# Kernel optimization log

Measured on AMD Instinct MI355X. Metric: run time of the kernel, lower is better.

The kernel has to match this reference:

```python
import jax, jax.numpy as jnp
import numpy as np

N_TOKENS, DIM = 4096, 2048
N_EXPERTS, TOPK, INTER = 32, 4, 1408
ALPHA, LIMIT, LIN_OFFSET = 1.702, 7.0, 1.0


def quick_geglu(h, probs):
    # h: [..., 2*INTER], interleaved gate/up as in the torch code (x[..., ::2], x[..., 1::2])
    gate = jnp.minimum(h[..., ::2], LIMIT)
    up = jnp.clip(h[..., 1::2], -LIMIT, LIMIT)
    glu = gate * jax.nn.sigmoid(ALPHA * gate)
    return glu * (up + LIN_OFFSET) * probs


def setup_inputs() -> dict:
    key = jax.random.key(0)
    k1, k2, k3, k4, k5 = jax.random.split(key, 5)
    x = jax.random.normal(k1, (N_TOKENS, DIM), dtype=jnp.float32)
    token_mask = jnp.ones((N_TOKENS,), dtype=bool)
    w = jax.random.uniform(k2, (N_TOKENS, TOPK), dtype=jnp.float32)
    weights = w / jnp.sum(w, axis=-1, keepdims=True)  # routing probs
    indices = jax.random.randint(k3, (N_TOKENS, TOPK), 0, N_EXPERTS, dtype=jnp.int64)
    gate_and_up_projs = 0.02 * jax.random.normal(k4, (N_EXPERTS, DIM, 2 * INTER), dtype=jnp.float32)
    down_projs = 0.02 * jax.random.normal(k5, (N_EXPERTS, INTER, DIM), dtype=jnp.float32)
    return {"x": x, "token_mask": token_mask, "weights": weights, "indices": indices,
            "gate_and_up_projs": gate_and_up_projs, "down_projs": down_projs}


def _moe_forward(x, weights, gup, down, token_mask, indices):
    N, D = x.shape
    E = gup.shape[0]
    topk = indices.shape[1]
    T = N * topk
    C = 2 * ((T + E - 1) // E)

    # masked tokens get expert id -1 (as in _permute_tokens_for_grouped_mm)
    flat_e = jnp.where(token_mask[:, None], indices, -1).reshape(-1)
    valid = flat_e >= 0
    e_id = jnp.where(valid, flat_e, E).astype(jnp.int32)  # invalid -> overflow group E
    w = jnp.where(valid, weights.reshape(-1).astype(jnp.float32), 0.0)
    tok = jnp.repeat(jnp.arange(N, dtype=jnp.int32), topk)

    # stable sort by expert (permutation step)
    order = jnp.argsort(e_id)
    se, st, sw = e_id[order], tok[order], w[order]

    # rank of each sorted assignment within its expert group
    counts = jnp.bincount(e_id, length=E + 1)
    starts = jnp.concatenate([jnp.zeros((1,), jnp.int32), jnp.cumsum(counts).astype(jnp.int32)])
    rank = jnp.arange(T, dtype=jnp.int32) - starts[se]
    valid_slot = (se < E) & (rank < C)
    dest = jnp.where(valid_slot, se * C + rank, E * C)  # overflow/dump row E*C

    # scatter permuted tokens into padded per-expert buffers [E, C, D]
    xb = jnp.zeros((E * C + 1, D), x.dtype).at[dest].set(x[st])
    pb = jnp.zeros((E * C + 1,), jnp.float32).at[dest].set(sw)
    tb = jnp.full((E * C + 1,), N, jnp.int32).at[dest].set(st)

    xg = xb[:E * C].reshape(E, C, D)
    h = jnp.einsum('ecd,edh->ech', xg, gup)                       # grouped gate+up GEMM
    a = quick_geglu(h, pb[:E * C].reshape(E, C, 1)).astype(x.dtype)  # fused act * probs
    y = jnp.einsum('ech,ehd->ecd', a, down).reshape(E * C, D)      # grouped down GEMM

    # combine: scatter-add back to token positions (empty slots have prob 0 -> y == 0)
    out = jnp.zeros((N + 1, D), x.dtype).at[tb[:E * C]].add(y)
    return out[:N]


def reference(x, token_mask, weights, indices, gate_and_up_projs, down_projs):
    return _moe_forward(x, weights, gate_and_up_projs, down_projs, token_mask, indices)
```

## Files before the change

kernel.cpp:

```cpp
#include <hip/hip_runtime.h>
#include <hip/hip_bf16.h>
#include <cstdint>
#include <cstddef>

#define N_TOKENS  4096
#define DIM       2048
#define N_EXPERTS 32
#define TOPK      4
#define INTER     1408
#define TWO_INTER 2816
#define CAP       1024
#define T_ASSIGN  (N_TOKENS*TOPK)
#define BK        32

typedef __attribute__((ext_vector_type(8))) short short8;
typedef __attribute__((ext_vector_type(4))) float f32x4;

__device__ __forceinline__ unsigned pack_bf16(float a, float b) {
  unsigned ua = __builtin_bit_cast(unsigned, a);
  unsigned ub = __builtin_bit_cast(unsigned, b);
  ua = (ua + 0x8000u) >> 16;
  ub = (ub + 0x8000u) & 0xFFFF0000u;
  return ua | ub;
}
__device__ __forceinline__ unsigned short bf16_1(float a) {
  return (unsigned short)((__builtin_bit_cast(unsigned, a) + 0x8000u) >> 16);
}
__device__ __forceinline__ float bf2f(unsigned u16) {
  return __builtin_bit_cast(float, u16 << 16);
}

__device__ __forceinline__ void gl_lds16(const void* g, void* l) {
  __builtin_amdgcn_global_load_lds(
      (const __attribute__((address_space(1))) unsigned int*)g,
      (__attribute__((address_space(3))) unsigned int*)l, 16, 0, 0);
}

__global__ void k_build(const int* __restrict__ tmask, const float* __restrict__ w,
                        const int* __restrict__ idx, int* __restrict__ counts,
                        int* __restrict__ tok, float* __restrict__ pb,
                        int* __restrict__ pos) {
  int i = blockIdx.x * 256 + threadIdx.x;
  if (i >= T_ASSIGN) return;
  int t = i >> 2;
  int e = idx[i];
  if (e < 0 || e >= N_EXPERTS) return;
  if (tmask[t] == 0) return;
  int r = atomicAdd(&counts[e], 1);
  if (r < CAP) {
    tok[e * CAP + r] = t;
    pb[e * CAP + r] = w[i];
    pos[i] = e * CAP + r;
  }
}

__global__ __launch_bounds__(256) void k_conv(const float* __restrict__ src,
                                              __hip_bfloat16* __restrict__ dst, int n4) {
  int i = blockIdx.x * 256 + threadIdx.x;
  int stride = gridDim.x * 256;
  for (; i < n4; i += stride) {
    float4 v = *(const float4*)(src + (size_t)i * 4);
    *(uint2*)(dst + (size_t)i * 4) = make_uint2(pack_bf16(v.x, v.y), pack_bf16(v.z, v.w));
  }
}

__global__ __launch_bounds__(256) void k_combine(const __hip_bfloat16* __restrict__ y,
                                                 const int* __restrict__ pos,
                                                 float* __restrict__ out) {
  int gid = blockIdx.x * 256 + threadIdx.x;
  int t  = gid >> 8;
  int c8 = (gid & 255) * 8;
  int4 p = *(const int4*)(pos + t * 4);
  float s[8] = {0.f, 0.f, 0.f, 0.f, 0.f, 0.f, 0.f, 0.f};
  #pragma unroll
  for (int k = 0; k < 4; ++k) {
    int pp = (k == 0) ? p.x : (k == 1) ? p.y : (k == 2) ? p.z : p.w;
    if (pp >= 0) {
      uint4 v = *(const uint4*)(y + (size_t)pp * DIM + c8);
      s[0] += bf2f(v.x & 0xffffu); s[1] += bf2f(v.x >> 16);
      s[2] += bf2f(v.y & 0xffffu); s[3] += bf2f(v.y >> 16);
      s[4] += bf2f(v.z & 0xffffu); s[5] += bf2f(v.z >> 16);
      s[6] += bf2f(v.w & 0xffffu); s[7] += bf2f(v.w >> 16);
    }
  }
  float* o = out + (size_t)t * DIM + c8;
  *(float4*)o       = make_float4(s[0], s[1], s[2], s[3]);
  *(float4*)(o + 4) = make_float4(s[4], s[5], s[6], s[7]);
}


#define STG(tt, KT) do {                                                     \
    if ((tt) < (KT)) {                                                       \
      char* base_ = smem + ((tt) & 1) * 32768;                               \
      const int ka_ = (tt) * BK;                                             \
      gl_lds16(aR0 + ka_, base_ + w * 2048 + lane * 16);                     \
      gl_lds16(aR1 + ka_, base_ + w * 2048 + 1024 + lane * 16);              \
      const size_t kb_ = (size_t)(tt) * BK * LDB;                            \
      gl_lds16(bR0 + kb_, base_ + 16384 + w * 1024 + lane * 16);             \
      gl_lds16(bR1 + kb_, base_ + 16384 + 8192 + w * 1024 + lane * 16);      \
    }                                                                        \
  } while (0)

#define KLOOP(KT) do {                                                       \
    STG(0, KT);                                                              \
    _Pragma("unroll 1")                                                      \
    for (int t = 0; t < (KT); ++t) {                                         \
      STG(t + 1, KT);                                                        \
      if (t + 1 < (KT)) { asm volatile("s_waitcnt vmcnt(4)" ::: "memory"); } \
      else             { asm volatile("s_waitcnt vmcnt(0)" ::: "memory"); }  \
      __builtin_amdgcn_s_barrier();                                          \
      const char* Ab_ = smem + (t & 1) * 32768;                              \
      const float* bq_ = (const float*)(Ab_ + 16384 + ((lane >> 4) << 3) * 512) \
                         + (wc * 64 + (lane & 15));                          \
      short8 af_[4];                                                         \
      _Pragma("unroll")                                                      \
      for (int mi_ = 0; mi_ < 4; ++mi_)                                      \
        af_[mi_] = *(const short8*)(Ab_ + (wr * 64 + mi_ * 16 + (lane & 15)) * 64 + rch); \
      _Pragma("unroll")                                                      \
      for (int ni_ = 0; ni_ < 4; ++ni_) {                                    \
        const float* q_ = bq_ + ni_ * 16;                                    \
        short8 bf_;                                                          \
        _Pragma("unroll")                                                    \
        for (int j_ = 0; j_ < 8; ++j_)                                       \
          bf_[j_] = (short)bf16_1(q_[j_ * 128]);                             \
        __builtin_amdgcn_s_setprio(1);                                       \
        _Pragma("unroll")                                                    \
        for (int mi_ = 0; mi_ < 4; ++mi_)                                    \
          acc[mi_][ni_] = __builtin_amdgcn_mfma_f32_16x16x32_bf16(           \
              af_[mi_], bf_, acc[mi_][ni_], 0, 0, 0);                        \
        __builtin_amdgcn_s_setprio(0);                                       \
      }                                                                      \
      __builtin_amdgcn_s_barrier();                                          \
    }                                                                        \
  } while (0)

__global__ __launch_bounds__(512, 4) void k_gemm1p(
    const __hip_bfloat16* __restrict__ xb, const float* __restrict__ gup,
    const int* __restrict__ counts, const int* __restrict__ tok,
    const float* __restrict__ pb, __hip_bfloat16* __restrict__ act,
    int* __restrict__ qh)
{
  __shared__ char smem[65536];
  __shared__ int s_item;
  const int NT = TWO_INTER / 128;
  const int KT = DIM / BK;
  const size_t LDB = TWO_INTER;
  const int xcd = blockIdx.x & 7;
  const int tid = threadIdx.x, lane = tid & 63, w = tid >> 6;
  const int wr = w >> 1, wc = w & 1;
  const int csw = ((lane & 3) ^ ((lane >> 3) & 3)) * 8;
  const int rch = (((lane >> 4) ^ ((lane >> 1) & 3)) << 4);
  const int rA0 = w * 32 + (lane >> 2);
  const int bk0 = tid >> 5;
  const int bn4 = (tid & 31) * 4;

  int mtcs[4], pre[5];
  pre[0] = 0;
  #pragma unroll
  for (int ei = 0; ei < 4; ++ei) {
    int cc = counts[xcd * 4 + ei]; cc = cc > CAP ? CAP : cc;
    mtcs[ei] = (cc + 255) >> 8;
    pre[ei + 1] = pre[ei] + NT * mtcs[ei];
  }
  const int total = pre[4];

  for (;;) {
    if (tid == 0) s_item = atomicAdd(&qh[xcd], 1);
    __syncthreads();
    const int it = s_item;
    if (it >= total) break;
    int ei = (it >= pre[1]) + (it >= pre[2]) + (it >= pre[3]);
    int loc = it - pre[ei];
    int mtc = mtcs[ei];
    int nt = loc / mtc, mt = loc - nt * mtc;
    const int e = xcd * 4 + ei;
    const int m0 = mt * 256, n0 = nt * 128;

    const float* gW = gup + (size_t)e * DIM * TWO_INTER + n0;
    const __hip_bfloat16* aR0 = xb + (size_t)tok[e * CAP + m0 + rA0] * DIM + csw;
    const __hip_bfloat16* aR1 = xb + (size_t)tok[e * CAP + m0 + rA0 + 16] * DIM + csw;
    const float* bR0 = gW + (size_t)bk0 * LDB + bn4;
    const float* bR1 = gW + (size_t)(bk0 + 16) * LDB + bn4;

    f32x4 acc[4][4];
    #pragma unroll
    for (int i = 0; i < 4; ++i)
      #pragma unroll
      for (int j = 0; j < 4; ++j) acc[i][j] = (f32x4){0.f, 0.f, 0.f, 0.f};

    KLOOP(KT);

    const int colp = lane & 15;
    const int rgrp = lane >> 4;
    #pragma unroll
    for (int mi = 0; mi < 4; ++mi) {
      #pragma unroll
      for (int j = 0; j < 4; ++j) {
        int rowl = wr * 64 + mi * 16 + rgrp * 4 + j;
        float prob = pb[e * CAP + m0 + rowl];
        size_t arow = (size_t)(e * CAP + m0 + rowl) * INTER;
        #pragma unroll
        for (int ni = 0; ni < 4; ++ni) {
          float v = acc[mi][ni][j];
          float other = __shfl_xor(v, 1, 64);
          if ((lane & 1) == 0) {
            float gate = fminf(v, 7.0f);
            float up   = fminf(fmaxf(other, -7.0f), 7.0f);
            float glu  = gate / (1.0f + __expf(-1.702f * gate));
            float a    = glu * (up + 1.0f) * prob;
            int nh = n0 + wc * 64 + ni * 16 + colp;
            act[arow + (nh >> 1)] = __float2bfloat16(a);
          }
        }
      }
    }
    __syncthreads();
  }
}

__global__ __launch_bounds__(512, 4) void k_gemm2p(
    const __hip_bfloat16* __restrict__ act, const float* __restrict__ down,
    const int* __restrict__ counts, __hip_bfloat16* __restrict__ y,
    int* __restrict__ qh)
{
  __shared__ char smem[65536];
  __shared__ int s_item;
  const int NT = DIM / 128;
  const int KT = INTER / BK;
  const size_t LDB = DIM;
  const int xcd = blockIdx.x & 7;
  const int tid = threadIdx.x, lane = tid & 63, w = tid >> 6;
  const int wr = w >> 1, wc = w & 1;
  const int csw = ((lane & 3) ^ ((lane >> 3) & 3)) * 8;
  const int rch = (((lane >> 4) ^ ((lane >> 1) & 3)) << 4);
  const int rA0 = w * 32 + (lane >> 2);
  const int bk0 = tid >> 5;
  const int bn4 = (tid & 31) * 4;

  int mtcs[4], pre[5];
  pre[0] = 0;
  #pragma unroll
  for (int ei = 0; ei < 4; ++ei) {
    int cc = counts[xcd * 4 + ei]; cc = cc > CAP ? CAP : cc;
    mtcs[ei] = (cc + 255) >> 8;
    pre[ei + 1] = pre[ei] + NT * mtcs[ei];
  }
  const int total = pre[4];

  for (;;) {
    if (tid == 0) s_item = atomicAdd(&qh[xcd], 1);
    __syncthreads();
    const int it = s_item;
    if (it >= total) break;
    int ei = (it >= pre[1]) + (it >= pre[2]) + (it >= pre[3]);
    int loc = it - pre[ei];
    int mtc = mtcs[ei];
    int nt = loc / mtc, mt = loc - nt * mtc;
    const int e = xcd * 4 + ei;
    const int m0 = mt * 256, n0 = nt * 128;

    const float* dW = down + (size_t)e * INTER * DIM + n0;
    const __hip_bfloat16* aR0 = act + (size_t)(e * CAP + m0 + rA0) * INTER + csw;
    const __hip_bfloat16* aR1 = act + (size_t)(e * CAP + m0 + rA0 + 16) * INTER + csw;
    const float* bR0 = dW + (size_t)bk0 * LDB + bn4;
    const float* bR1 = dW + (size_t)(bk0 + 16) * LDB + bn4;

    f32x4 acc[4][4];
    #pragma unroll
    for (int i = 0; i < 4; ++i)
      #pragma unroll
      for (int j = 0; j < 4; ++j) acc[i][j] = (f32x4){0.f, 0.f, 0.f, 0.f};

    KLOOP(KT);

    const int colp = lane & 15;
    const int rgrp = lane >> 4;
    #pragma unroll
    for (int mi = 0; mi < 4; ++mi) {
      #pragma unroll
      for (int j = 0; j < 4; ++j) {
        int rowl = wr * 64 + mi * 16 + rgrp * 4 + j;
        __hip_bfloat16* yrow = y + (size_t)(e * CAP + m0 + rowl) * DIM + n0;
        #pragma unroll
        for (int ni = 0; ni < 4; ++ni)
          yrow[wc * 64 + ni * 16 + colp] = __float2bfloat16(acc[mi][ni][j]);
      }
    }
    __syncthreads();
  }
}


extern "C" void kernel_launch(void* const* d_in, const int* in_sizes, int n_in,
                              void* d_out, int out_size, void* d_ws, size_t ws_size,
                              hipStream_t stream) {
  const float* x     = (const float*)d_in[0];
  const int*   tmask = (const int*)d_in[1];
  const float* w     = (const float*)d_in[2];
  const int*   idx   = (const int*)d_in[3];
  const float* gup   = (const float*)d_in[4];
  const float* down  = (const float*)d_in[5];
  float* out = (float*)d_out;

  char* ws = (char*)d_ws;
  const size_t off_qh1   = 128;
  const size_t off_qh2   = 160;
  const size_t off_tok   = 256;
  const size_t off_pb    = off_tok + 131072;
  const size_t off_pos   = off_pb + 131072;
  const size_t off_act   = off_pos + 65536;
  const size_t act_bytes = (size_t)N_EXPERTS * CAP * INTER * 2;
  const size_t off_xb    = off_act + act_bytes;
  const size_t xb_bytes  = (size_t)N_TOKENS * DIM * 2;
  const size_t off_y     = off_xb + xb_bytes;

  int*   counts = (int*)ws;
  int*   qh1    = (int*)(ws + off_qh1);
  int*   qh2    = (int*)(ws + off_qh2);
  int*   tok    = (int*)(ws + off_tok);
  float* pbuf   = (float*)(ws + off_pb);
  int*   pos    = (int*)(ws + off_pos);
  __hip_bfloat16* act = (__hip_bfloat16*)(ws + off_act);
  __hip_bfloat16* xb  = (__hip_bfloat16*)(ws + off_xb);
  __hip_bfloat16* y   = (__hip_bfloat16*)(ws + off_y);

  hipMemsetAsync(ws, 0, off_pos, stream);
  hipMemsetAsync(ws + off_pos, 0xFF, 65536, stream);
  k_build<<<(T_ASSIGN + 255) / 256, 256, 0, stream>>>(tmask, w, idx, counts, tok, pbuf, pos);

  k_conv<<<2048, 256, 0, stream>>>(x, xb, (N_TOKENS * DIM) / 4);

  k_gemm1p<<<512, 512, 0, stream>>>(xb, gup, counts, tok, pbuf, act, qh1);
  k_gemm2p<<<512, 512, 0, stream>>>(act, down, counts, y, qh2);
  k_combine<<<N_TOKENS, 256, 0, stream>>>(y, pos, out);
}
```

Before: 802.5 us.

## Register-prefetch fp32 weights and convert once to swizzled bf16 LDS tiles

Instead of staging fp32 weight tiles into LDS with async global-to-LDS loads and converting every element per wave at MFMA time, each thread now loads its 8 fp32 weights two tiles ahead into registers, packs them to bf16 once, and stores one swizzled 16-byte chunk to a smaller double-buffered LDS region. MFMA operands for B are then read as plain short8 LDS loads. The intent is to remove redundant per-wave conversions and scalar strided LDS reads, and to halve the B LDS footprint. In exchange it uses more registers, adds an lgkmcnt wait and a register-to-LDS store each step, and the weight global loads become 4-byte strided per-lane loads.

```diff
diff --git a/kernel.cpp b/kernel.cpp
--- a/kernel.cpp
+++ b/kernel.cpp
@@ -22,9 +22,6 @@
   ua = (ua + 0x8000u) >> 16;
   ub = (ub + 0x8000u) & 0xFFFF0000u;
   return ua | ub;
-}
-__device__ __forceinline__ unsigned short bf16_1(float a) {
-  return (unsigned short)((__builtin_bit_cast(unsigned, a) + 0x8000u) >> 16);
 }
 __device__ __forceinline__ float bf2f(unsigned u16) {
   return __builtin_bit_cast(float, u16 << 16);
@@ -89,49 +86,65 @@
 }
 
 
-#define STG(tt, KT) do {                                                     \
-    if ((tt) < (KT)) {                                                       \
-      char* base_ = smem + ((tt) & 1) * 32768;                               \
-      const int ka_ = (tt) * BK;                                             \
-      gl_lds16(aR0 + ka_, base_ + w * 2048 + lane * 16);                     \
-      gl_lds16(aR1 + ka_, base_ + w * 2048 + 1024 + lane * 16);              \
-      const size_t kb_ = (size_t)(tt) * BK * LDB;                            \
-      gl_lds16(bR0 + kb_, base_ + 16384 + w * 1024 + lane * 16);             \
-      gl_lds16(bR1 + kb_, base_ + 16384 + 8192 + w * 1024 + lane * 16);      \
-    }                                                                        \
+#define TILE_STEP(t, bcur, KT, LDB) do {                                    \
+    if ((t) + 1 < (KT)) {                                                   \
+      char* ad_ = smem + (((t) + 1) & 1) * 16384 + w * 2048 + lane * 16;    \
+      gl_lds16(aP0 + (size_t)((t) + 1) * BK, ad_);                          \
+      gl_lds16(aP1 + (size_t)((t) + 1) * BK, ad_ + 1024);                   \
+      asm volatile("s_waitcnt vmcnt(10)" ::: "memory");                     \
+    } else {                                                                \
+      asm volatile("s_waitcnt vmcnt(0)" ::: "memory");                      \
+    }                                                                       \
+    { uint4 u_;                                                             \
+      u_.x = pack_bf16(bcur[0], bcur[1]);                                   \
+      u_.y = pack_bf16(bcur[2], bcur[3]);                                   \
+      u_.z = pack_bf16(bcur[4], bcur[5]);                                   \
+      u_.w = pack_bf16(bcur[6], bcur[7]);                                   \
+      *(uint4*)(bbf + ((t) & 1) * 8192 + bwoff) = u_; }                     \
+    if ((t) + 2 < (KT)) {                                                   \
+      const float* p_ = bG + (size_t)((t) + 2) * BK * (LDB);                \
+      _Pragma("unroll")                                                     \
+      for (int j_ = 0; j_ < 8; ++j_) bcur[j_] = p_[(size_t)j_ * (LDB)];     \
+    }                                                                       \
+    asm volatile("s_waitcnt lgkmcnt(0)" ::: "memory");                      \
+    __builtin_amdgcn_s_barrier();                                           \
+    __builtin_amdgcn_sched_barrier(0);                                      \
+    { const char* Ab_ = smem + ((t) & 1) * 16384;                           \
+      const char* Bb_ = bbf + ((t) & 1) * 8192;                             \
+      short8 af_[4], bf_[4];                                                \
+      _Pragma("unroll")                                                     \
+      for (int mi_ = 0; mi_ < 4; ++mi_)                                     \
+        af_[mi_] = *(const short8*)(Ab_ + (wr * 64 + mi_ * 16 + (lane & 15)) * 64 + rch); \
+      _Pragma("unroll")                                                     \
+      for (int ni_ = 0; ni_ < 4; ++ni_)                                     \
+        bf_[ni_] = *(const short8*)(Bb_ + (wc * 64 + ni_ * 16 + (lane & 15)) * 64 + rch); \
+      __builtin_amdgcn_s_setprio(1);                                        \
+      _Pragma("unroll")                                                     \
+      for (int mi_ = 0; mi_ < 4; ++mi_)                                     \
+        _Pragma("unroll")                                                   \
+        for (int ni_ = 0; ni_ < 4; ++ni_)                                   \
+          acc[mi_][ni_] = __builtin_amdgcn_mfma_f32_16x16x32_bf16(          \
+              af_[mi_], bf_[ni_], acc[mi_][ni_], 0, 0, 0);                  \
+      __builtin_amdgcn_s_setprio(0); }                                      \
+    __builtin_amdgcn_s_barrier();                                           \
   } while (0)
 
-#define KLOOP(KT) do {                                                       \
-    STG(0, KT);                                                              \
-    _Pragma("unroll 1")                                                      \
-    for (int t = 0; t < (KT); ++t) {                                         \
-      STG(t + 1, KT);                                                        \
-      if (t + 1 < (KT)) { asm volatile("s_waitcnt vmcnt(4)" ::: "memory"); } \
-      else             { asm volatile("s_waitcnt vmcnt(0)" ::: "memory"); }  \
-      __builtin_amdgcn_s_barrier();                                          \
-      const char* Ab_ = smem + (t & 1) * 32768;                              \
-      const float* bq_ = (const float*)(Ab_ + 16384 + ((lane >> 4) << 3) * 512) \
-                         + (wc * 64 + (lane & 15));                          \
-      short8 af_[4];                                                         \
-      _Pragma("unroll")                                                      \
-      for (int mi_ = 0; mi_ < 4; ++mi_)                                      \
-        af_[mi_] = *(const short8*)(Ab_ + (wr * 64 + mi_ * 16 + (lane & 15)) * 64 + rch); \
-      _Pragma("unroll")                                                      \
-      for (int ni_ = 0; ni_ < 4; ++ni_) {                                    \
-        const float* q_ = bq_ + ni_ * 16;                                    \
-        short8 bf_;                                                          \
-        _Pragma("unroll")                                                    \
-        for (int j_ = 0; j_ < 8; ++j_)                                       \
-          bf_[j_] = (short)bf16_1(q_[j_ * 128]);                             \
-        __builtin_amdgcn_s_setprio(1);                                       \
-        _Pragma("unroll")                                                    \
-        for (int mi_ = 0; mi_ < 4; ++mi_)                                    \
-          acc[mi_][ni_] = __builtin_amdgcn_mfma_f32_16x16x32_bf16(           \
-              af_[mi_], bf_, acc[mi_][ni_], 0, 0, 0);                        \
-        __builtin_amdgcn_s_setprio(0);                                       \
-      }                                                                      \
-      __builtin_amdgcn_s_barrier();                                          \
-    }                                                                        \
+#define GKLOOP(KT, LDB) do {                                                \
+    {                                                                       \
+      char* ad0_ = smem + w * 2048 + lane * 16;                             \
+      gl_lds16(aP0, ad0_);                                                  \
+      gl_lds16(aP1, ad0_ + 1024);                                           \
+      _Pragma("unroll")                                                     \
+      for (int j_ = 0; j_ < 8; ++j_) bE[j_] = bG[(size_t)j_ * (LDB)];       \
+      const float* p1_ = bG + (size_t)BK * (LDB);                           \
+      _Pragma("unroll")                                                     \
+      for (int j_ = 0; j_ < 8; ++j_) bO[j_] = p1_[(size_t)j_ * (LDB)];      \
+    }                                                                       \
+    _Pragma("unroll 1")                                                     \
+    for (int t = 0; t < (KT); t += 2) {                                     \
+      TILE_STEP(t,     bE, (KT), (LDB));                                    \
+      TILE_STEP(t + 1, bO, (KT), (LDB));                                    \
+    }                                                                       \
   } while (0)
 
 __global__ __launch_bounds__(512, 4) void k_gemm1p(
@@ -140,19 +153,20 @@
     const float* __restrict__ pb, __hip_bfloat16* __restrict__ act,
     int* __restrict__ qh)
 {
-  __shared__ char smem[65536];
+  __shared__ char smem[49152];
   __shared__ int s_item;
+  char* bbf = smem + 32768;
   const int NT = TWO_INTER / 128;
   const int KT = DIM / BK;
-  const size_t LDB = TWO_INTER;
   const int xcd = blockIdx.x & 7;
   const int tid = threadIdx.x, lane = tid & 63, w = tid >> 6;
   const int wr = w >> 1, wc = w & 1;
   const int csw = ((lane & 3) ^ ((lane >> 3) & 3)) * 8;
   const int rch = (((lane >> 4) ^ ((lane >> 1) & 3)) << 4);
   const int rA0 = w * 32 + (lane >> 2);
-  const int bk0 = tid >> 5;
-  const int bn4 = (tid & 31) * 4;
+  const int bn  = tid & 127;
+  const int bkc = tid >> 7;
+  const int bwoff = bn * 64 + ((bkc ^ ((bn >> 1) & 3)) << 4);
 
   int mtcs[4], pre[5];
   pre[0] = 0;
@@ -176,19 +190,19 @@
     const int e = xcd * 4 + ei;
     const int m0 = mt * 256, n0 = nt * 128;
 
-    const float* gW = gup + (size_t)e * DIM * TWO_INTER + n0;
-    const __hip_bfloat16* aR0 = xb + (size_t)tok[e * CAP + m0 + rA0] * DIM + csw;
-    const __hip_bfloat16* aR1 = xb + (size_t)tok[e * CAP + m0 + rA0 + 16] * DIM + csw;
-    const float* bR0 = gW + (size_t)bk0 * LDB + bn4;
-    const float* bR1 = gW + (size_t)(bk0 + 16) * LDB + bn4;
+    const float* gW = gup + (size_t)e * DIM * TWO_INTER;
+    const __hip_bfloat16* aP0 = xb + (size_t)tok[e * CAP + m0 + rA0] * DIM + csw;
+    const __hip_bfloat16* aP1 = xb + (size_t)tok[e * CAP + m0 + rA0 + 16] * DIM + csw;
+    const float* bG = gW + (size_t)(bkc * 8) * TWO_INTER + n0 + bn;
 
     f32x4 acc[4][4];
     #pragma unroll
     for (int i = 0; i < 4; ++i)
       #pragma unroll
       for (int j = 0; j < 4; ++j) acc[i][j] = (f32x4){0.f, 0.f, 0.f, 0.f};
-
-    KLOOP(KT);
+    float bE[8], bO[8];
+
+    GKLOOP(KT, TWO_INTER);
 
     const int colp = lane & 15;
     const int rgrp = lane >> 4;
@@ -223,19 +237,20 @@
     const int* __restrict__ counts, __hip_bfloat16* __restrict__ y,
     int* __restrict__ qh)
 {
-  __shared__ char smem[65536];
+  __shared__ char smem[49152];
   __shared__ int s_item;
+  char* bbf = smem + 32768;
   const int NT = DIM / 128;
   const int KT = INTER / BK;
-  const size_t LDB = DIM;
   const int xcd = blockIdx.x & 7;
   const int tid = threadIdx.x, lane = tid & 63, w = tid >> 6;
   const int wr = w >> 1, wc = w & 1;
   const int csw = ((lane & 3) ^ ((lane >> 3) & 3)) * 8;
   const int rch = (((lane >> 4) ^ ((lane >> 1) & 3)) << 4);
   const int rA0 = w * 32 + (lane >> 2);
-  const int bk0 = tid >> 5;
-  const int bn4 = (tid & 31) * 4;
+  const int bn  = tid & 127;
+  const int bkc = tid >> 7;
+  const int bwoff = bn * 64 + ((bkc ^ ((bn >> 1) & 3)) << 4);
 
   int mtcs[4], pre[5];
   pre[0] = 0;
@@ -259,19 +274,19 @@
     const int e = xcd * 4 + ei;
     const int m0 = mt * 256, n0 = nt * 128;
 
-    const float* dW = down + (size_t)e * INTER * DIM + n0;
-    const __hip_bfloat16* aR0 = act + (size_t)(e * CAP + m0 + rA0) * INTER + csw;
-    const __hip_bfloat16* aR1 = act + (size_t)(e * CAP + m0 + rA0 + 16) * INTER + csw;
-    const float* bR0 = dW + (size_t)bk0 * LDB + bn4;
-    const float* bR1 = dW + (size_t)(bk0 + 16) * LDB + bn4;
+    const float* dW = down + (size_t)e * INTER * DIM;
+    const __hip_bfloat16* aP0 = act + (size_t)(e * CAP + m0 + rA0) * INTER + csw;
+    const __hip_bfloat16* aP1 = act + (size_t)(e * CAP + m0 + rA0 + 16) * INTER + csw;
+    const float* bG = dW + (size_t)(bkc * 8) * DIM + n0 + bn;
 
     f32x4 acc[4][4];
     #pragma unroll
     for (int i = 0; i < 4; ++i)
       #pragma unroll
       for (int j = 0; j < 4; ++j) acc[i][j] = (f32x4){0.f, 0.f, 0.f, 0.f};
-
-    KLOOP(KT);
+    float bE[8], bO[8];
+
+    GKLOOP(KT, DIM);
 
     const int colp = lane & 15;
     const int rgrp = lane >> 4;
```

Measured after the change: 705.2 us. -12.1%, faster.
